# Optimization experiments

Hardware: AMD Instinct MI355X
Metric: run time of the kernel (lower is better)

The kernel has to match this reference:

```python
import jax, jax.numpy as jnp
import numpy as np

G, C, L, D, H, NCLS = 64, 32, 128, 64, 128, 10


def setup_inputs() -> dict:
    key = jax.random.key(0)
    ks = jax.random.split(key, 5)
    scale = 0.05
    return {
        "cycle_reps": jax.random.normal(ks[0], (G, C, L, D), dtype=jnp.float32),
        "W_ih": jax.random.normal(ks[1], (4 * H, D), dtype=jnp.float32) * scale,
        "W_hh": jax.random.normal(ks[2], (4 * H, H), dtype=jnp.float32) * scale,
        "b_ih": jnp.zeros((4 * H,), dtype=jnp.float32),
        "b_hh": jnp.zeros((4 * H,), dtype=jnp.float32),
        "W_cls": jax.random.normal(ks[3], (NCLS, H), dtype=jnp.float32) * scale,
        "b_cls": jnp.zeros((NCLS,), dtype=jnp.float32),
    }


def _lstm_seq_sum(x, W_ih, W_hh, b):
    """Run a single-layer LSTM over x [B, L, D]; return sum of hidden states over L -> [B, H]."""
    B = x.shape[0]
    Hh = W_hh.shape[1]
    # precompute input-side gate pre-activations for all timesteps: [L, B, 4H]
    xg = jnp.einsum('bld,gd->lbg', x, W_ih) + b

    def step(carry, xg_t):
        h, c = carry
        gates = xg_t + h @ W_hh.T  # [B, 4H]
        i, f, g, o = jnp.split(gates, 4, axis=-1)  # torch i/f/g/o gate order
        i = jax.nn.sigmoid(i)
        f = jax.nn.sigmoid(f)
        g = jnp.tanh(g)
        o = jax.nn.sigmoid(o)
        c = f * c + i * g
        h = o * jnp.tanh(c)
        return (h, c), h

    init = (jnp.zeros((B, Hh), x.dtype), jnp.zeros((B, Hh), x.dtype))
    _, hs = jax.lax.scan(step, init, xg)  # hs: [L, B, H]
    return hs.sum(axis=0)


def reference(cycle_reps, W_ih, W_hh, b_ih, b_hh, W_cls, b_cls):
    Gn, Cn, Ln, Dn = cycle_reps.shape
    x = cycle_reps.reshape(Gn * Cn, Ln, Dn)
    rep = _lstm_seq_sum(x, W_ih, W_hh, b_ih + b_hh)  # [G*C, H]: sum of LSTM outputs over seq
    rep = rep.reshape(Gn, Cn, -1)
    # torch.var_mean over the cycle axis; only the mean is used as the graph rep
    graph_mean = rep.mean(axis=1)  # [G, H]
    logits = graph_mean @ W_cls.T + b_cls  # classifier_gnn
    return jax.nn.log_softmax(logits, axis=1)
```

## Files before the change

kernel.cpp:

```cpp
#include <hip/hip_runtime.h>
#include <hip/hip_bf16.h>

#define NSEQ 2048
#define LSEQ 128
#define DIN  64
#define HID  128
#define NCLS 10
#define XPAD 72
#define CHK  16

typedef __attribute__((ext_vector_type(8))) short bfrag8;
typedef __attribute__((ext_vector_type(4))) float facc4;

__device__ __forceinline__ short f2bf(float f) {
    union { __hip_bfloat16 b; short s; } u;
    u.b = __float2bfloat16(f);
    return u.s;
}

__device__ __forceinline__ bfrag8 load_bf16_frag(const float* __restrict__ p) {
    bfrag8 r;
#pragma unroll
    for (int j = 0; j < 8; ++j) r[j] = f2bf(p[j]);
    return r;
}

__device__ __forceinline__ float fast_sigmoid(float x) {
    float e = __builtin_amdgcn_exp2f(-1.4426950408889634f * x);
    return __builtin_amdgcn_rcpf(1.0f + e);
}
__device__ __forceinline__ float fast_tanh(float x) {
    float e = __builtin_amdgcn_exp2f(2.8853900817779268f * x);
    return 1.0f - 2.0f * __builtin_amdgcn_rcpf(1.0f + e);
}

__global__ __launch_bounds__(512) void lstm_fused(
    const float* __restrict__ x,
    const float* __restrict__ Wih,
    const float* __restrict__ Whh,
    const float* __restrict__ bih,
    const float* __restrict__ bhh,
    float* __restrict__ rep)
{
    __shared__ __align__(16) __hip_bfloat16 hbuf[2][16][136];
    __shared__ __align__(16) __hip_bfloat16 xs[2][CHK][8][XPAD];

    const int tid  = threadIdx.x;
    const int w    = tid >> 6;
    const int lane = tid & 63;
    const int ln   = lane & 15;
    const int qd   = lane >> 4;
    const int s0   = blockIdx.x * 8;
    const int khid = w * 16 + ln;

    bfrag8 whh[4][4];
    bfrag8 wih[4][2];
    float  biasv[4];
#pragma unroll
    for (int g = 0; g < 4; ++g) {
        const int col = g * HID + khid;
        biasv[g] = bih[col] + bhh[col];
#pragma unroll
        for (int k0 = 0; k0 < 4; ++k0)
            whh[g][k0] = load_bf16_frag(Whh + col * HID + k0 * 32 + qd * 8);
#pragma unroll
        for (int k0 = 0; k0 < 2; ++k0)
            wih[g][k0] = load_bf16_frag(Wih + col * DIN + k0 * 32 + qd * 8);
    }

    {
        unsigned int* p = (unsigned int*)&hbuf[0][0][0];
        for (int i = tid; i < 2 * 16 * 136 / 2; i += 512) p[i] = 0u;
    }

    const float* xsrc = x + (size_t)(s0 + w) * (LSEQ * DIN) + lane * 16;
    const int stt = lane >> 2;
    const int sdd = (lane & 3) * 16;

    {
        float4 l0 = ((const float4*)xsrc)[0];
        float4 l1 = ((const float4*)xsrc)[1];
        float4 l2 = ((const float4*)xsrc)[2];
        float4 l3 = ((const float4*)xsrc)[3];
        bfrag8 o0, o1;
#pragma unroll
        for (int j = 0; j < 4; ++j) { o0[j] = f2bf(((float*)&l0)[j]); o0[4+j] = f2bf(((float*)&l1)[j]); }
#pragma unroll
        for (int j = 0; j < 4; ++j) { o1[j] = f2bf(((float*)&l2)[j]); o1[4+j] = f2bf(((float*)&l3)[j]); }
        *(bfrag8*)&xs[0][stt][w][sdd]     = o0;
        *(bfrag8*)&xs[0][stt][w][sdd + 8] = o1;
    }

    float cst[4]  = {0.f, 0.f, 0.f, 0.f};
    float hsum[4] = {0.f, 0.f, 0.f, 0.f};

    __syncthreads();

    int cur = 0;
    for (int chunk = 0; chunk < LSEQ / CHK; ++chunk) {
        const int buf = chunk & 1;
        const bool more = chunk < (LSEQ / CHK - 1);
        float4 l0, l1, l2, l3;
#pragma unroll 1
        for (int ct = 0; ct < CHK; ++ct) {
            bfrag8 hf[4];
#pragma unroll
            for (int k0 = 0; k0 < 4; ++k0)
                hf[k0] = *(const bfrag8*)(&hbuf[cur][ln][k0 * 32 + qd * 8]);
            bfrag8 xf0 = *(const bfrag8*)(&xs[buf][ct][ln & 7][qd * 8]);
            bfrag8 xf1 = *(const bfrag8*)(&xs[buf][ct][ln & 7][32 + qd * 8]);

            if (ct == 0 && more) {
                const float* p = xsrc + (chunk + 1) * (CHK * DIN);
                l0 = ((const float4*)p)[0];
                l1 = ((const float4*)p)[1];
                l2 = ((const float4*)p)[2];
                l3 = ((const float4*)p)[3];
            }
            if (ct == 12 && more) {
                bfrag8 o0, o1;
#pragma unroll
                for (int j = 0; j < 4; ++j) { o0[j] = f2bf(((float*)&l0)[j]); o0[4+j] = f2bf(((float*)&l1)[j]); }
#pragma unroll
                for (int j = 0; j < 4; ++j) { o1[j] = f2bf(((float*)&l2)[j]); o1[4+j] = f2bf(((float*)&l3)[j]); }
                *(bfrag8*)&xs[buf ^ 1][stt][w][sdd]     = o0;
                *(bfrag8*)&xs[buf ^ 1][stt][w][sdd + 8] = o1;
            }

            facc4 acc[4];
#pragma unroll
            for (int g = 0; g < 4; ++g)
                acc[g] = (facc4){biasv[g], biasv[g], biasv[g], biasv[g]};
#pragma unroll
            for (int g = 0; g < 4; ++g) {
                acc[g] = __builtin_amdgcn_mfma_f32_16x16x32_bf16(xf0, wih[g][0], acc[g], 0, 0, 0);
                acc[g] = __builtin_amdgcn_mfma_f32_16x16x32_bf16(xf1, wih[g][1], acc[g], 0, 0, 0);
            }
#pragma unroll
            for (int g = 0; g < 4; ++g)
#pragma unroll
                for (int k0 = 0; k0 < 4; ++k0)
                    acc[g] = __builtin_amdgcn_mfma_f32_16x16x32_bf16(hf[k0], whh[g][k0], acc[g], 0, 0, 0);

            short hb[4];
#pragma unroll
            for (int r = 0; r < 4; ++r) {
                float iv = fast_sigmoid(acc[0][r]);
                float fv = fast_sigmoid(acc[1][r]);
                float gv = fast_tanh(acc[2][r]);
                float ov = fast_sigmoid(acc[3][r]);
                float c  = fv * cst[r] + iv * gv;
                cst[r]   = c;
                float hv = ov * fast_tanh(c);
                hsum[r] += hv;
                hb[r]    = f2bf(hv);
            }

            if (qd < 2) {
#pragma unroll
                for (int r = 0; r < 4; ++r)
                    ((short*)&hbuf[cur ^ 1][qd * 4 + r][0])[khid] = hb[r];
            }
            __syncthreads();
            cur ^= 1;
        }
    }

    if (qd < 2) {
#pragma unroll
        for (int r = 0; r < 4; ++r)
            rep[(size_t)(s0 + qd * 4 + r) * HID + khid] = hsum[r];
    }
}

__global__ __launch_bounds__(128) void cls_kernel(
    const float* __restrict__ rep,
    const float* __restrict__ Wcls,
    const float* __restrict__ bcls,
    float* __restrict__ out)
{
    __shared__ float m_s[HID];
    __shared__ float logits_s[NCLS];
    const int g = blockIdx.x;
    const int h = threadIdx.x;

    float s = 0.f;
#pragma unroll 4
    for (int c = 0; c < 32; ++c)
        s += rep[((size_t)g * 32 + c) * HID + h];
    m_s[h] = s * (1.0f / 32.0f);
    __syncthreads();

    if (h < NCLS) {
        float acc = bcls[h];
        for (int k = 0; k < HID; ++k)
            acc += m_s[k] * Wcls[h * HID + k];
        logits_s[h] = acc;
    }
    __syncthreads();

    if (h < NCLS) {
        float mx = logits_s[0];
#pragma unroll
        for (int j = 1; j < NCLS; ++j) mx = fmaxf(mx, logits_s[j]);
        float se = 0.f;
#pragma unroll
        for (int j = 0; j < NCLS; ++j)
            se += __builtin_amdgcn_exp2f((logits_s[j] - mx) * 1.4426950408889634f);
        float lse = mx + 0.6931471805599453f * __builtin_amdgcn_logf(se);
        out[g * NCLS + h] = logits_s[h] - lse;
    }
}

extern "C" void kernel_launch(void* const* d_in, const int* in_sizes, int n_in,
                              void* d_out, int out_size, void* d_ws, size_t ws_size,
                              hipStream_t stream) {
    const float* x    = (const float*)d_in[0];
    const float* Wih  = (const float*)d_in[1];
    const float* Whh  = (const float*)d_in[2];
    const float* bih  = (const float*)d_in[3];
    const float* bhh  = (const float*)d_in[4];
    const float* Wcls = (const float*)d_in[5];
    const float* bcls = (const float*)d_in[6];

    float* rep = (float*)d_ws;

    lstm_fused<<<NSEQ / 8, 512, 0, stream>>>(x, Wih, Whh, bih, bhh, rep);
    cls_kernel<<<64, 128, 0, stream>>>(rep, Wcls, bcls, (float*)d_out);
}
```

Before: 231.1 us.

## Software-pipeline input projection and split gate math across all lanes

```diff
diff --git a/kernel.cpp b/kernel.cpp
--- a/kernel.cpp
+++ b/kernel.cpp
@@ -52,6 +52,9 @@
     const int qd   = lane >> 4;
     const int s0   = blockIdx.x * 8;
     const int khid = w * 16 + ln;
+    const int sq0  = (qd & 1) * 4 + (qd >> 1) * 2;
+    const int sq1  = sq0 + 1;
+    const bool hi  = (qd >= 2);
 
     bfrag8 whh[4][4];
     bfrag8 wih[4][2];
@@ -78,99 +81,125 @@
     const int sdd = (lane & 3) * 16;
 
     {
-        float4 l0 = ((const float4*)xsrc)[0];
-        float4 l1 = ((const float4*)xsrc)[1];
-        float4 l2 = ((const float4*)xsrc)[2];
-        float4 l3 = ((const float4*)xsrc)[3];
+        float4 a0 = ((const float4*)xsrc)[0];
+        float4 a1 = ((const float4*)xsrc)[1];
+        float4 a2 = ((const float4*)xsrc)[2];
+        float4 a3 = ((const float4*)xsrc)[3];
         bfrag8 o0, o1;
 #pragma unroll
-        for (int j = 0; j < 4; ++j) { o0[j] = f2bf(((float*)&l0)[j]); o0[4+j] = f2bf(((float*)&l1)[j]); }
-#pragma unroll
-        for (int j = 0; j < 4; ++j) { o1[j] = f2bf(((float*)&l2)[j]); o1[4+j] = f2bf(((float*)&l3)[j]); }
+        for (int j = 0; j < 4; ++j) { o0[j] = f2bf(((float*)&a0)[j]); o0[4+j] = f2bf(((float*)&a1)[j]); }
+#pragma unroll
+        for (int j = 0; j < 4; ++j) { o1[j] = f2bf(((float*)&a2)[j]); o1[4+j] = f2bf(((float*)&a3)[j]); }
         *(bfrag8*)&xs[0][stt][w][sdd]     = o0;
         *(bfrag8*)&xs[0][stt][w][sdd + 8] = o1;
     }
 
-    float cst[4]  = {0.f, 0.f, 0.f, 0.f};
-    float hsum[4] = {0.f, 0.f, 0.f, 0.f};
+    float cst[2]  = {0.f, 0.f};
+    float hsum[2] = {0.f, 0.f};
 
     __syncthreads();
 
+    facc4 accA[4], accB[4];
+    {
+        bfrag8 x0 = *(const bfrag8*)(&xs[0][0][ln & 7][qd * 8]);
+        bfrag8 x1 = *(const bfrag8*)(&xs[0][0][ln & 7][32 + qd * 8]);
+#pragma unroll
+        for (int g = 0; g < 4; ++g) {
+            accA[g] = (facc4){biasv[g], biasv[g], biasv[g], biasv[g]};
+            accA[g] = __builtin_amdgcn_mfma_f32_16x16x32_bf16(x0, wih[g][0], accA[g], 0, 0, 0);
+            accA[g] = __builtin_amdgcn_mfma_f32_16x16x32_bf16(x1, wih[g][1], accA[g], 0, 0, 0);
+        }
+    }
+
     int cur = 0;
+
+#define STEP(ACCIN, ACCOUT, CT)                                                          \
+    {                                                                                    \
+        const int ct = (CT);                                                             \
+                                             \
+        bfrag8 hf[4];                                                                    \
+        _Pragma("unroll")                                                                \
+        for (int k0 = 0; k0 < 4; ++k0)                                                   \
+            hf[k0] = *(const bfrag8*)(&hbuf[cur][ln][k0 * 32 + qd * 8]);                 \
+             \
+        const int nbuf = (ct < CHK - 1) ? buf : (buf ^ 1);                               \
+        const int nct  = (ct + 1) & (CHK - 1);                                           \
+        bfrag8 xf0 = *(const bfrag8*)(&xs[nbuf][nct][ln & 7][qd * 8]);                   \
+        bfrag8 xf1 = *(const bfrag8*)(&xs[nbuf][nct][ln & 7][32 + qd * 8]);              \
+                    \
+        _Pragma("unroll")                                                                \
+        for (int g = 0; g < 4; ++g)                                                      \
+            _Pragma("unroll")                                                            \
+            for (int k0 = 0; k0 < 4; ++k0)                                               \
+                ACCIN[g] = __builtin_amdgcn_mfma_f32_16x16x32_bf16(hf[k0], whh[g][k0], ACCIN[g], 0, 0, 0); \
+                \
+        float rc2[4], rc3[4];                                                            \
+        _Pragma("unroll")                                                                \
+        for (int g = 0; g < 4; ++g) {                                                    \
+            rc2[g] = __shfl_xor(ACCIN[g][2], 32);                                        \
+            rc3[g] = __shfl_xor(ACCIN[g][3], 32);                                        \
+        }                                                                                \
+                              \
+        _Pragma("unroll")                                                                \
+        for (int g = 0; g < 4; ++g) {                                                    \
+            ACCOUT[g] = (facc4){biasv[g], biasv[g], biasv[g], biasv[g]};                 \
+            ACCOUT[g] = __builtin_amdgcn_mfma_f32_16x16x32_bf16(xf0, wih[g][0], ACCOUT[g], 0, 0, 0); \
+            ACCOUT[g] = __builtin_amdgcn_mfma_f32_16x16x32_bf16(xf1, wih[g][1], ACCOUT[g], 0, 0, 0); \
+        }                                                                                \
+        if (ct == 0 && more) {                      \
+            const float* p = xsrc + (chunk + 1) * (CHK * DIN);                           \
+            l0 = ((const float4*)p)[0];                                                  \
+            l1 = ((const float4*)p)[1];                                                  \
+            l2 = ((const float4*)p)[2];                                                  \
+            l3 = ((const float4*)p)[3];                                                  \
+        }                                                                                \
+        if (ct == 12 && more) {                   \
+            bfrag8 o0, o1;                                                               \
+            _Pragma("unroll")                                                            \
+            for (int j = 0; j < 4; ++j) { o0[j] = f2bf(((float*)&l0)[j]); o0[4+j] = f2bf(((float*)&l1)[j]); } \
+            _Pragma("unroll")                                                            \
+            for (int j = 0; j < 4; ++j) { o1[j] = f2bf(((float*)&l2)[j]); o1[4+j] = f2bf(((float*)&l3)[j]); } \
+            *(bfrag8*)&xs[buf ^ 1][stt][w][sdd]     = o0;                                \
+            *(bfrag8*)&xs[buf ^ 1][stt][w][sdd + 8] = o1;                                \
+        }                                                                                \
+                               \
+        short hb[2];                                                                     \
+        _Pragma("unroll")                                                                \
+        for (int j = 0; j < 2; ++j) {                                                    \
+            float u0 = hi ? (j ? rc3[0] : rc2[0]) : ACCIN[0][j];                         \
+            float u1 = hi ? (j ? rc3[1] : rc2[1]) : ACCIN[1][j];                         \
+            float u2 = hi ? (j ? rc3[2] : rc2[2]) : ACCIN[2][j];                         \
+            float u3 = hi ? (j ? rc3[3] : rc2[3]) : ACCIN[3][j];                         \
+            float iv = fast_sigmoid(u0);                                                 \
+            float fv = fast_sigmoid(u1);                                                 \
+            float gv = fast_tanh(u2);                                                    \
+            float ov = fast_sigmoid(u3);                                                 \
+            float c  = fv * cst[j] + iv * gv;                                            \
+            cst[j]   = c;                                                                \
+            float hv = ov * fast_tanh(c);                                                \
+            hsum[j] += hv;                                                               \
+            hb[j]    = f2bf(hv);                                                         \
+        }                                                                                \
+        ((short*)&hbuf[cur ^ 1][sq0][0])[khid] = hb[0];                                  \
+        ((short*)&hbuf[cur ^ 1][sq1][0])[khid] = hb[1];                                  \
+        __syncthreads();                                                                 \
+        cur ^= 1;                                                                        \
+    }
+
     for (int chunk = 0; chunk < LSEQ / CHK; ++chunk) {
         const int buf = chunk & 1;
         const bool more = chunk < (LSEQ / CHK - 1);
         float4 l0, l1, l2, l3;
 #pragma unroll 1
-        for (int ct = 0; ct < CHK; ++ct) {
-            bfrag8 hf[4];
-#pragma unroll
-            for (int k0 = 0; k0 < 4; ++k0)
-                hf[k0] = *(const bfrag8*)(&hbuf[cur][ln][k0 * 32 + qd * 8]);
-            bfrag8 xf0 = *(const bfrag8*)(&xs[buf][ct][ln & 7][qd * 8]);
-            bfrag8 xf1 = *(const bfrag8*)(&xs[buf][ct][ln & 7][32 + qd * 8]);
-
-            if (ct == 0 && more) {
-                const float* p = xsrc + (chunk + 1) * (CHK * DIN);
-                l0 = ((const float4*)p)[0];
-                l1 = ((const float4*)p)[1];
-                l2 = ((const float4*)p)[2];
-                l3 = ((const float4*)p)[3];
-            }
-            if (ct == 12 && more) {
-                bfrag8 o0, o1;
-#pragma unroll
-                for (int j = 0; j < 4; ++j) { o0[j] = f2bf(((float*)&l0)[j]); o0[4+j] = f2bf(((float*)&l1)[j]); }
-#pragma unroll
-                for (int j = 0; j < 4; ++j) { o1[j] = f2bf(((float*)&l2)[j]); o1[4+j] = f2bf(((float*)&l3)[j]); }
-                *(bfrag8*)&xs[buf ^ 1][stt][w][sdd]     = o0;
-                *(bfrag8*)&xs[buf ^ 1][stt][w][sdd + 8] = o1;
-            }
-
-            facc4 acc[4];
-#pragma unroll
-            for (int g = 0; g < 4; ++g)
-                acc[g] = (facc4){biasv[g], biasv[g], biasv[g], biasv[g]};
-#pragma unroll
-            for (int g = 0; g < 4; ++g) {
-                acc[g] = __builtin_amdgcn_mfma_f32_16x16x32_bf16(xf0, wih[g][0], acc[g], 0, 0, 0);
-                acc[g] = __builtin_amdgcn_mfma_f32_16x16x32_bf16(xf1, wih[g][1], acc[g], 0, 0, 0);
-            }
-#pragma unroll
-            for (int g = 0; g < 4; ++g)
-#pragma unroll
-                for (int k0 = 0; k0 < 4; ++k0)
-                    acc[g] = __builtin_amdgcn_mfma_f32_16x16x32_bf16(hf[k0], whh[g][k0], acc[g], 0, 0, 0);
-
-            short hb[4];
-#pragma unroll
-            for (int r = 0; r < 4; ++r) {
-                float iv = fast_sigmoid(acc[0][r]);
-                float fv = fast_sigmoid(acc[1][r]);
-                float gv = fast_tanh(acc[2][r]);
-                float ov = fast_sigmoid(acc[3][r]);
-                float c  = fv * cst[r] + iv * gv;
-                cst[r]   = c;
-                float hv = ov * fast_tanh(c);
-                hsum[r] += hv;
-                hb[r]    = f2bf(hv);
-            }
-
-            if (qd < 2) {
-#pragma unroll
-                for (int r = 0; r < 4; ++r)
-                    ((short*)&hbuf[cur ^ 1][qd * 4 + r][0])[khid] = hb[r];
-            }
-            __syncthreads();
-            cur ^= 1;
+        for (int ct2 = 0; ct2 < CHK / 2; ++ct2) {
+            STEP(accA, accB, 2 * ct2);
+            STEP(accB, accA, 2 * ct2 + 1);
         }
     }
-
-    if (qd < 2) {
-#pragma unroll
-        for (int r = 0; r < 4; ++r)
-            rep[(size_t)(s0 + qd * 4 + r) * HID + khid] = hsum[r];
-    }
+#undef STEP
+
+    rep[(size_t)(s0 + sq0) * HID + khid] = hsum[0];
+    rep[(size_t)(s0 + sq1) * HID + khid] = hsum[1];
 }
 
 __global__ __launch_bounds__(128) void cls_kernel(
```

After: 201.3 us. 1.15x faster.
